# Kernel optimization log

Hardware: AMD Instinct MI355X
Metric: run time of the kernel (lower is better)

## Reference

```python
import jax, jax.numpy as jnp
import numpy as np
import math

B, S, H, D = 2, 2048, 16, 64  # batch, seq, heads, head_dim (hidden=1024)


def setup_inputs() -> dict:
    key = jax.random.key(0)
    kq, kk, kv, kb, km = jax.random.split(key, 5)
    q = jax.random.normal(kq, (B, S, H, D), dtype=jnp.float32)
    k = jax.random.normal(kk, (B, S, H, D), dtype=jnp.float32)
    v = jax.random.normal(kv, (B, S, H, D), dtype=jnp.float32)
    attn_bias = jax.random.normal(kb, (B, H, S, S), dtype=jnp.float32)
    mask = jax.random.randint(km, (B, S, S), 0, 2).astype(jnp.bool_)
    return {"q": q, "k": k, "v": v, "attn_bias": attn_bias, "mask": mask}


def reference(q, k, v, attn_bias, mask):
    # Faithful to CoreAttention: q is MULTIPLIED by sqrt(d_head),
    # masked positions in the score matrix are filled with 0 (not -inf),
    # dropout rate is 0 (identity).
    scale = math.sqrt(D)
    # scores: [B, H, S, S]
    x = jnp.einsum('bshd,bthd->bhst', q * scale, k)
    x = x + attn_bias
    x = jnp.where(mask[:, None, :, :], jnp.float32(0.0), x)  # masked_fill(mask, 0)
    x = jax.nn.softmax(x, axis=-1)
    out = jnp.einsum('bhst,bthd->bshd', x, v)  # [B, S, H, D]
    return out.reshape(B, S, H * D)
```

## Files before the change

### kernel.cpp

```cpp
#include <hip/hip_runtime.h>
#include <math.h>


namespace {
constexpr int Bn = 2, Sn = 2048, Hn = 16, Dn = 64;
constexpr int QT = 64;
constexpr int KT = 64;
constexpr int ST = 72;

typedef _Float16 f16x8 __attribute__((ext_vector_type(8)));
typedef float    f32x4 __attribute__((ext_vector_type(4)));
}

__global__ __launch_bounds__(256, 4)
void core_attn_kernel(const float* __restrict__ Q,
                      const float* __restrict__ K,
                      const float* __restrict__ V,
                      const float* __restrict__ Bias,
                      const int*   __restrict__ Mask,
                      float* __restrict__ Out)
{
    const int qt = blockIdx.x;
    const int h  = blockIdx.y;
    const int b  = blockIdx.z;
    const int q0 = qt * QT;

    const int tid  = threadIdx.x;
    const int wave = tid >> 6;
    const int lane = tid & 63;
    const int c    = lane & 15;
    const int quad = lane >> 4;

    __shared__ __align__(16) _Float16 Khi[KT * ST];
    __shared__ __align__(16) _Float16 Klo[KT * ST];
    __shared__ __align__(16) _Float16 Vt [Dn * ST];
    __shared__ __align__(16) _Float16 Pl [4][16 * ST];

    f16x8 qhi[2], qlo[2];
    {
        const int qrow = q0 + wave * 16 + c;
        const float* qp = Q + ((size_t)((b * Sn + qrow) * Hn + h)) * Dn + quad * 8;
        #pragma unroll
        for (int kc = 0; kc < 2; ++kc) {
            float4 v0 = *(const float4*)(qp + kc * 32);
            float4 v1 = *(const float4*)(qp + kc * 32 + 4);
            float buf[8] = {v0.x, v0.y, v0.z, v0.w, v1.x, v1.y, v1.z, v1.w};
            #pragma unroll
            for (int j = 0; j < 8; ++j) {
                float f = buf[j] * 8.0f;
                _Float16 hi = (_Float16)f;
                qhi[kc][j] = hi;
                qlo[kc][j] = (_Float16)(f - (float)hi);
            }
        }
    }

    f32x4 Oa[4];
    float m_i[4], l_i[4];
    #pragma unroll
    for (int r = 0; r < 4; ++r) { m_i[r] = -INFINITY; l_i[r] = 0.0f; }
    #pragma unroll
    for (int t = 0; t < 4; ++t) Oa[t] = (f32x4){0.f, 0.f, 0.f, 0.f};

    const float* bias_row = Bias + ((size_t)(b * Hn + h) * Sn + (q0 + wave * 16 + quad * 4)) * Sn;
    const int*   mask_row = Mask + ((size_t)(b * Sn + (q0 + wave * 16 + quad * 4))) * Sn;

    const int srow = tid >> 2;
    const int dseg = (tid & 3) * 16;
    const float* kbase = K + ((size_t)((b * Sn + srow) * Hn + h)) * Dn + dseg;
    const float* vbase = V + ((size_t)((b * Sn + srow) * Hn + h)) * Dn + dseg;

    for (int k0 = 0; k0 < Sn; k0 += KT) {
        __syncthreads();
        {
            const float* kp = kbase + (size_t)k0 * (Hn * Dn);
            const float* vp = vbase + (size_t)k0 * (Hn * Dn);
            float4 kv[4], vv[4];
            #pragma unroll
            for (int i = 0; i < 4; ++i) kv[i] = *(const float4*)(kp + 4 * i);
            #pragma unroll
            for (int i = 0; i < 4; ++i) vv[i] = *(const float4*)(vp + 4 * i);
            f16x8 khiv[2], klov[2];
            const float* kf = (const float*)kv;
            #pragma unroll
            for (int j = 0; j < 16; ++j) {
                float f = kf[j];
                _Float16 hi = (_Float16)f;
                khiv[j >> 3][j & 7] = hi;
                klov[j >> 3][j & 7] = (_Float16)(f - (float)hi);
            }
            *(f16x8*)&Khi[srow * ST + dseg]     = khiv[0];
            *(f16x8*)&Khi[srow * ST + dseg + 8] = khiv[1];
            *(f16x8*)&Klo[srow * ST + dseg]     = klov[0];
            *(f16x8*)&Klo[srow * ST + dseg + 8] = klov[1];
            const float* vf = (const float*)vv;
            #pragma unroll
            for (int j = 0; j < 16; ++j)
                Vt[(dseg + j) * ST + srow] = (_Float16)vf[j];
        }
        __syncthreads();

        float sc[4][4];
        #pragma unroll
        for (int ct = 0; ct < 4; ++ct) {
            f32x4 acc;
            #pragma unroll
            for (int r = 0; r < 4; ++r)
                acc[r] = bias_row[(size_t)r * Sn + k0 + ct * 16 + c];
            #pragma unroll
            for (int kc = 0; kc < 2; ++kc) {
                f16x8 kh = *(const f16x8*)&Khi[(ct * 16 + c) * ST + kc * 32 + quad * 8];
                f16x8 kl = *(const f16x8*)&Klo[(ct * 16 + c) * ST + kc * 32 + quad * 8];
                acc = __builtin_amdgcn_mfma_f32_16x16x32_f16(qhi[kc], kh, acc, 0, 0, 0);
                acc = __builtin_amdgcn_mfma_f32_16x16x32_f16(qhi[kc], kl, acc, 0, 0, 0);
                acc = __builtin_amdgcn_mfma_f32_16x16x32_f16(qlo[kc], kh, acc, 0, 0, 0);
            }
            #pragma unroll
            for (int r = 0; r < 4; ++r) {
                int mv = mask_row[(size_t)r * Sn + k0 + ct * 16 + c];
                sc[ct][r] = mv ? 0.0f : acc[r];
            }
        }

        float mt[4];
        #pragma unroll
        for (int r = 0; r < 4; ++r)
            mt[r] = fmaxf(fmaxf(sc[0][r], sc[1][r]), fmaxf(sc[2][r], sc[3][r]));
        #pragma unroll
        for (int off = 8; off >= 1; off >>= 1) {
            #pragma unroll
            for (int r = 0; r < 4; ++r)
                mt[r] = fmaxf(mt[r], __shfl_xor(mt[r], off, 64));
        }
        float alpha[4], rs[4];
        #pragma unroll
        for (int r = 0; r < 4; ++r) {
            float mn = fmaxf(m_i[r], mt[r]);
            alpha[r] = __expf(m_i[r] - mn);
            m_i[r] = mn;
            rs[r] = 0.0f;
        }
        #pragma unroll
        for (int ct = 0; ct < 4; ++ct) {
            #pragma unroll
            for (int r = 0; r < 4; ++r) {
                float p = __expf(sc[ct][r] - m_i[r]);
                sc[ct][r] = p;
                rs[r] += p;
            }
        }
        #pragma unroll
        for (int off = 8; off >= 1; off >>= 1) {
            #pragma unroll
            for (int r = 0; r < 4; ++r)
                rs[r] += __shfl_xor(rs[r], off, 64);
        }
        #pragma unroll
        for (int r = 0; r < 4; ++r)
            l_i[r] = l_i[r] * alpha[r] + rs[r];
        #pragma unroll
        for (int t = 0; t < 4; ++t) {
            #pragma unroll
            for (int r = 0; r < 4; ++r)
                Oa[t][r] *= alpha[r];
        }

        #pragma unroll
        for (int ct = 0; ct < 4; ++ct) {
            #pragma unroll
            for (int r = 0; r < 4; ++r)
                Pl[wave][(quad * 4 + r) * ST + ct * 16 + c] = (_Float16)sc[ct][r];
        }
        f16x8 pf[2];
        #pragma unroll
        for (int kc = 0; kc < 2; ++kc)
            pf[kc] = *(const f16x8*)&Pl[wave][c * ST + kc * 32 + quad * 8];

        #pragma unroll
        for (int td = 0; td < 4; ++td) {
            #pragma unroll
            for (int kc = 0; kc < 2; ++kc) {
                f16x8 vfrag = *(const f16x8*)&Vt[(td * 16 + c) * ST + kc * 32 + quad * 8];
                Oa[td] = __builtin_amdgcn_mfma_f32_16x16x32_f16(pf[kc], vfrag, Oa[td], 0, 0, 0);
            }
        }
    }

    #pragma unroll
    for (int r = 0; r < 4; ++r) l_i[r] = 1.0f / l_i[r];
    float* op = Out + ((size_t)(b * Sn + q0 + wave * 16 + quad * 4)) * (Hn * Dn) + h * Dn + c;
    #pragma unroll
    for (int td = 0; td < 4; ++td) {
        #pragma unroll
        for (int r = 0; r < 4; ++r)
            op[(size_t)r * (Hn * Dn) + td * 16] = Oa[td][r] * l_i[r];
    }
}

extern "C" void kernel_launch(void* const* d_in, const int* in_sizes, int n_in,
                              void* d_out, int out_size, void* d_ws, size_t ws_size,
                              hipStream_t stream) {
    const float* q    = (const float*)d_in[0];
    const float* k    = (const float*)d_in[1];
    const float* v    = (const float*)d_in[2];
    const float* bias = (const float*)d_in[3];
    const int*   mask = (const int*)d_in[4];
    float* out = (float*)d_out;

    dim3 grid(Sn / QT, Hn, Bn);
    core_attn_kernel<<<grid, 256, 0, stream>>>(q, k, v, bias, mask, out);
}
```

Baseline: 919.3 us.

## Prefetch next tile into registers, transpose MFMA operands for vectorized bias/mask loads

Register-prefetches the next K/V tile, bias and mask while the current tile computes, so global latency overlaps compute. It swaps the MFMA A/B operands so each lane owns one query row. Bias and mask then load as contiguous float4/int4 non-temporal loads, and row reductions shrink to two shuffles. It also remaps block indices for L2 locality, vectorizes the V transpose, P stores and output stores, and adds register pressure that may cut occupancy.

```diff
diff --git a/kernel.cpp b/kernel.cpp
--- a/kernel.cpp
+++ b/kernel.cpp
@@ -6,10 +6,13 @@
 constexpr int Bn = 2, Sn = 2048, Hn = 16, Dn = 64;
 constexpr int QT = 64;
 constexpr int KT = 64;
+constexpr int NT = Sn / KT;
 constexpr int ST = 72;
 
 typedef _Float16 f16x8 __attribute__((ext_vector_type(8)));
+typedef _Float16 f16x4 __attribute__((ext_vector_type(4)));
 typedef float    f32x4 __attribute__((ext_vector_type(4)));
+typedef int      i32x4 __attribute__((ext_vector_type(4)));
 }
 
 __global__ __launch_bounds__(256, 4)
@@ -20,9 +23,12 @@
                       const int*   __restrict__ Mask,
                       float* __restrict__ Out)
 {
-    const int qt = blockIdx.x;
-    const int h  = blockIdx.y;
-    const int b  = blockIdx.z;
+    const int p  = blockIdx.x + 32 * (blockIdx.y + 16 * blockIdx.z);
+    const int sl = p >> 3;
+    const int g  = (p & 7) + 8 * (sl >> 5);
+    const int qt = sl & 31;
+    const int h  = g & 15;
+    const int b  = g >> 4;
     const int q0 = qt * QT;
 
     const int tid  = threadIdx.x;
@@ -36,15 +42,16 @@
     __shared__ __align__(16) _Float16 Vt [Dn * ST];
     __shared__ __align__(16) _Float16 Pl [4][16 * ST];
 
+    const int qrow = q0 + wave * 16 + c;
+
     f16x8 qhi[2], qlo[2];
     {
-        const int qrow = q0 + wave * 16 + c;
         const float* qp = Q + ((size_t)((b * Sn + qrow) * Hn + h)) * Dn + quad * 8;
         #pragma unroll
         for (int kc = 0; kc < 2; ++kc) {
-            float4 v0 = *(const float4*)(qp + kc * 32);
-            float4 v1 = *(const float4*)(qp + kc * 32 + 4);
-            float buf[8] = {v0.x, v0.y, v0.z, v0.w, v1.x, v1.y, v1.z, v1.w};
+            f32x4 v0 = *(const f32x4*)(qp + kc * 32);
+            f32x4 v1 = *(const f32x4*)(qp + kc * 32 + 4);
+            float buf[8] = {v0[0], v0[1], v0[2], v0[3], v1[0], v1[1], v1[2], v1[3]};
             #pragma unroll
             for (int j = 0; j < 8; ++j) {
                 float f = buf[j] * 8.0f;
@@ -55,121 +62,136 @@
         }
     }
 
+    const float* bias_base = Bias + ((size_t)(b * Hn + h) * Sn + qrow) * Sn + quad * 4;
+    const int*   mask_base = Mask + ((size_t)b * Sn + qrow) * Sn + quad * 4;
+
+    const int ksrow = tid >> 2;
+    const int kdseg = (tid & 3) * 16;
+    const float* kbase = K + ((size_t)((b * Sn + ksrow) * Hn + h)) * Dn + kdseg;
+    const int vkq = tid >> 4;
+    const int vdq = (tid & 15) * 4;
+    const float* vbase = V + ((size_t)((b * Sn + vkq * 4) * Hn + h)) * Dn + vdq;
+
+    f32x4 kreg[4], vreg[4], breg[4];
+    i32x4 mreg[4];
+
+    auto issue_kv = [&](int k0) {
+        const float* kp = kbase + (size_t)k0 * (Hn * Dn);
+        const float* vp = vbase + (size_t)k0 * (Hn * Dn);
+        #pragma unroll
+        for (int i = 0; i < 4; ++i) kreg[i] = *(const f32x4*)(kp + 4 * i);
+        #pragma unroll
+        for (int i = 0; i < 4; ++i) vreg[i] = *(const f32x4*)(vp + (size_t)i * (Hn * Dn));
+    };
+    auto issue_b = [&](int k0) {
+        #pragma unroll
+        for (int ct = 0; ct < 4; ++ct)
+            breg[ct] = __builtin_nontemporal_load((const f32x4*)(bias_base + k0 + ct * 16));
+    };
+    auto issue_m = [&](int k0) {
+        #pragma unroll
+        for (int ct = 0; ct < 4; ++ct)
+            mreg[ct] = __builtin_nontemporal_load((const i32x4*)(mask_base + k0 + ct * 16));
+    };
+    auto stage = [&]() {
+        f16x8 khiv[2], klov[2];
+        const float* kf = (const float*)kreg;
+        #pragma unroll
+        for (int j = 0; j < 16; ++j) {
+            float f = kf[j];
+            _Float16 hi = (_Float16)f;
+            khiv[j >> 3][j & 7] = hi;
+            klov[j >> 3][j & 7] = (_Float16)(f - (float)hi);
+        }
+        *(f16x8*)&Khi[ksrow * ST + kdseg]     = khiv[0];
+        *(f16x8*)&Khi[ksrow * ST + kdseg + 8] = khiv[1];
+        *(f16x8*)&Klo[ksrow * ST + kdseg]     = klov[0];
+        *(f16x8*)&Klo[ksrow * ST + kdseg + 8] = klov[1];
+        #pragma unroll
+        for (int j = 0; j < 4; ++j) {
+            f16x4 w;
+            #pragma unroll
+            for (int i = 0; i < 4; ++i) w[i] = (_Float16)vreg[i][j];
+            *(f16x4*)&Vt[(vdq + j) * ST + vkq * 4] = w;
+        }
+    };
+
     f32x4 Oa[4];
-    float m_i[4], l_i[4];
     #pragma unroll
-    for (int r = 0; r < 4; ++r) { m_i[r] = -INFINITY; l_i[r] = 0.0f; }
-    #pragma unroll
-    for (int t = 0; t < 4; ++t) Oa[t] = (f32x4){0.f, 0.f, 0.f, 0.f};
-
-    const float* bias_row = Bias + ((size_t)(b * Hn + h) * Sn + (q0 + wave * 16 + quad * 4)) * Sn;
-    const int*   mask_row = Mask + ((size_t)(b * Sn + (q0 + wave * 16 + quad * 4))) * Sn;
-
-    const int srow = tid >> 2;
-    const int dseg = (tid & 3) * 16;
-    const float* kbase = K + ((size_t)((b * Sn + srow) * Hn + h)) * Dn + dseg;
-    const float* vbase = V + ((size_t)((b * Sn + srow) * Hn + h)) * Dn + dseg;
-
-    for (int k0 = 0; k0 < Sn; k0 += KT) {
+    for (int td = 0; td < 4; ++td) Oa[td] = (f32x4){0.f, 0.f, 0.f, 0.f};
+    float m_i = -INFINITY, l_i = 0.0f;
+
+    issue_kv(0);
+    issue_b(0);
+    issue_m(0);
+    stage();
+
+    for (int t = 0; t < NT; ++t) {
         __syncthreads();
-        {
-            const float* kp = kbase + (size_t)k0 * (Hn * Dn);
-            const float* vp = vbase + (size_t)k0 * (Hn * Dn);
-            float4 kv[4], vv[4];
-            #pragma unroll
-            for (int i = 0; i < 4; ++i) kv[i] = *(const float4*)(kp + 4 * i);
-            #pragma unroll
-            for (int i = 0; i < 4; ++i) vv[i] = *(const float4*)(vp + 4 * i);
-            f16x8 khiv[2], klov[2];
-            const float* kf = (const float*)kv;
-            #pragma unroll
-            for (int j = 0; j < 16; ++j) {
-                float f = kf[j];
-                _Float16 hi = (_Float16)f;
-                khiv[j >> 3][j & 7] = hi;
-                klov[j >> 3][j & 7] = (_Float16)(f - (float)hi);
-            }
-            *(f16x8*)&Khi[srow * ST + dseg]     = khiv[0];
-            *(f16x8*)&Khi[srow * ST + dseg + 8] = khiv[1];
-            *(f16x8*)&Klo[srow * ST + dseg]     = klov[0];
-            *(f16x8*)&Klo[srow * ST + dseg + 8] = klov[1];
-            const float* vf = (const float*)vv;
-            #pragma unroll
-            for (int j = 0; j < 16; ++j)
-                Vt[(dseg + j) * ST + srow] = (_Float16)vf[j];
-        }
-        __syncthreads();
-
-        float sc[4][4];
-        #pragma unroll
-        for (int ct = 0; ct < 4; ++ct) {
-            f32x4 acc;
-            #pragma unroll
-            for (int r = 0; r < 4; ++r)
-                acc[r] = bias_row[(size_t)r * Sn + k0 + ct * 16 + c];
+        const int k0n = (t + 1) * KT;
+
+        f32x4 acc[4];
+        #pragma unroll
+        for (int ct = 0; ct < 4; ++ct) acc[ct] = breg[ct];
+        if (t + 1 < NT) issue_b(k0n);
+
+        #pragma unroll
+        for (int ct = 0; ct < 4; ++ct) {
             #pragma unroll
             for (int kc = 0; kc < 2; ++kc) {
                 f16x8 kh = *(const f16x8*)&Khi[(ct * 16 + c) * ST + kc * 32 + quad * 8];
                 f16x8 kl = *(const f16x8*)&Klo[(ct * 16 + c) * ST + kc * 32 + quad * 8];
-                acc = __builtin_amdgcn_mfma_f32_16x16x32_f16(qhi[kc], kh, acc, 0, 0, 0);
-                acc = __builtin_amdgcn_mfma_f32_16x16x32_f16(qhi[kc], kl, acc, 0, 0, 0);
-                acc = __builtin_amdgcn_mfma_f32_16x16x32_f16(qlo[kc], kh, acc, 0, 0, 0);
-            }
+                acc[ct] = __builtin_amdgcn_mfma_f32_16x16x32_f16(kh, qhi[kc], acc[ct], 0, 0, 0);
+                acc[ct] = __builtin_amdgcn_mfma_f32_16x16x32_f16(kh, qlo[kc], acc[ct], 0, 0, 0);
+                acc[ct] = __builtin_amdgcn_mfma_f32_16x16x32_f16(kl, qhi[kc], acc[ct], 0, 0, 0);
+            }
+        }
+
+        float sc[4][4];
+        #pragma unroll
+        for (int ct = 0; ct < 4; ++ct) {
+            #pragma unroll
+            for (int r = 0; r < 4; ++r)
+                sc[ct][r] = mreg[ct][r] ? 0.0f : acc[ct][r];
+        }
+        if (t + 1 < NT) { issue_m(k0n); issue_kv(k0n); }
+
+        float mt = sc[0][0];
+        #pragma unroll
+        for (int ct = 0; ct < 4; ++ct) {
+            #pragma unroll
+            for (int r = 0; r < 4; ++r) mt = fmaxf(mt, sc[ct][r]);
+        }
+        mt = fmaxf(mt, __shfl_xor(mt, 16, 64));
+        mt = fmaxf(mt, __shfl_xor(mt, 32, 64));
+        float mn = fmaxf(m_i, mt);
+        float alpha = __expf(m_i - mn);
+        m_i = mn;
+        float rs = 0.0f;
+        #pragma unroll
+        for (int ct = 0; ct < 4; ++ct) {
             #pragma unroll
             for (int r = 0; r < 4; ++r) {
-                int mv = mask_row[(size_t)r * Sn + k0 + ct * 16 + c];
-                sc[ct][r] = mv ? 0.0f : acc[r];
-            }
-        }
-
-        float mt[4];
-        #pragma unroll
-        for (int r = 0; r < 4; ++r)
-            mt[r] = fmaxf(fmaxf(sc[0][r], sc[1][r]), fmaxf(sc[2][r], sc[3][r]));
-        #pragma unroll
-        for (int off = 8; off >= 1; off >>= 1) {
-            #pragma unroll
-            for (int r = 0; r < 4; ++r)
-                mt[r] = fmaxf(mt[r], __shfl_xor(mt[r], off, 64));
-        }
-        float alpha[4], rs[4];
-        #pragma unroll
-        for (int r = 0; r < 4; ++r) {
-            float mn = fmaxf(m_i[r], mt[r]);
-            alpha[r] = __expf(m_i[r] - mn);
-            m_i[r] = mn;
-            rs[r] = 0.0f;
-        }
-        #pragma unroll
-        for (int ct = 0; ct < 4; ++ct) {
-            #pragma unroll
-            for (int r = 0; r < 4; ++r) {
-                float p = __expf(sc[ct][r] - m_i[r]);
-                sc[ct][r] = p;
-                rs[r] += p;
-            }
-        }
-        #pragma unroll
-        for (int off = 8; off >= 1; off >>= 1) {
-            #pragma unroll
-            for (int r = 0; r < 4; ++r)
-                rs[r] += __shfl_xor(rs[r], off, 64);
-        }
-        #pragma unroll
-        for (int r = 0; r < 4; ++r)
-            l_i[r] = l_i[r] * alpha[r] + rs[r];
-        #pragma unroll
-        for (int t = 0; t < 4; ++t) {
-            #pragma unroll
-            for (int r = 0; r < 4; ++r)
-                Oa[t][r] *= alpha[r];
-        }
-
-        #pragma unroll
-        for (int ct = 0; ct < 4; ++ct) {
-            #pragma unroll
-            for (int r = 0; r < 4; ++r)
-                Pl[wave][(quad * 4 + r) * ST + ct * 16 + c] = (_Float16)sc[ct][r];
+                float pe = __expf(sc[ct][r] - mn);
+                sc[ct][r] = pe;
+                rs += pe;
+            }
+        }
+        rs += __shfl_xor(rs, 16, 64);
+        rs += __shfl_xor(rs, 32, 64);
+        l_i = l_i * alpha + rs;
+        #pragma unroll
+        for (int td = 0; td < 4; ++td) {
+            #pragma unroll
+            for (int r = 0; r < 4; ++r) Oa[td][r] *= alpha;
+        }
+
+        #pragma unroll
+        for (int ct = 0; ct < 4; ++ct) {
+            f16x4 w;
+            #pragma unroll
+            for (int r = 0; r < 4; ++r) w[r] = (_Float16)sc[ct][r];
+            *(f16x4*)&Pl[wave][c * ST + ct * 16 + quad * 4] = w;
         }
         f16x8 pf[2];
         #pragma unroll
@@ -180,20 +202,25 @@
         for (int td = 0; td < 4; ++td) {
             #pragma unroll
             for (int kc = 0; kc < 2; ++kc) {
-                f16x8 vfrag = *(const f16x8*)&Vt[(td * 16 + c) * ST + kc * 32 + quad * 8];
-                Oa[td] = __builtin_amdgcn_mfma_f32_16x16x32_f16(pf[kc], vfrag, Oa[td], 0, 0, 0);
-            }
+                f16x8 vf = *(const f16x8*)&Vt[(td * 16 + c) * ST + kc * 32 + quad * 8];
+                Oa[td] = __builtin_amdgcn_mfma_f32_16x16x32_f16(vf, pf[kc], Oa[td], 0, 0, 0);
+            }
+        }
+
+        if (t + 1 < NT) {
+            __syncthreads();
+            stage();
         }
     }
 
-    #pragma unroll
-    for (int r = 0; r < 4; ++r) l_i[r] = 1.0f / l_i[r];
-    float* op = Out + ((size_t)(b * Sn + q0 + wave * 16 + quad * 4)) * (Hn * Dn) + h * Dn + c;
+    const float inv = 1.0f / l_i;
+    float* op = Out + ((size_t)(b * Sn + qrow)) * (Hn * Dn) + h * Dn + quad * 4;
     #pragma unroll
     for (int td = 0; td < 4; ++td) {
-        #pragma unroll
-        for (int r = 0; r < 4; ++r)
-            op[(size_t)r * (Hn * Dn) + td * 16] = Oa[td][r] * l_i[r];
+        f32x4 o;
+        #pragma unroll
+        for (int r = 0; r < 4; ++r) o[r] = Oa[td][r] * inv;
+        __builtin_nontemporal_store(o, (f32x4*)(op + td * 16));
     }
 }
 
```

Result: slower. 942.2 us (+2.5%).
